# Kernel tuning notes

Measured on AMD Instinct MI355X. Metric: run time of the kernel, lower is better.

Reference implementation:

```python
import jax, jax.numpy as jnp
import numpy as np

N_NODES = 100000
N_EDGES = 600000
D = 128  # input_dim == output_dim (required by index_add into zeros_like(x) + residual)
EPS = 1e-5


def _linear_params(key, d_in, d_out):
    kw, kb = jax.random.split(key)
    bound = 1.0 / np.sqrt(d_in)
    w = jax.random.uniform(kw, (d_in, d_out), minval=-bound, maxval=bound, dtype=jnp.float32)
    b = jax.random.uniform(kb, (d_out,), minval=-bound, maxval=bound, dtype=jnp.float32)
    return w, b


def setup_inputs() -> dict:
    key = jax.random.key(0)
    ks = jax.random.split(key, 6)
    x = jax.random.normal(ks[0], (N_NODES, D), dtype=jnp.float32)
    edge_index = jax.random.randint(ks[1], (2, N_EDGES), 0, N_NODES, dtype=jnp.int32)
    w_m1, b_m1 = _linear_params(ks[2], 2 * D, D)
    w_m2, b_m2 = _linear_params(ks[3], D, D)
    w_u1, b_u1 = _linear_params(ks[4], 2 * D, D)
    w_u2, b_u2 = _linear_params(ks[5], D, D)
    gamma = jnp.ones((D,), dtype=jnp.float32)
    beta = jnp.zeros((D,), dtype=jnp.float32)
    return {
        "x": x, "edge_index": edge_index,
        "w_m1": w_m1, "b_m1": b_m1, "w_m2": w_m2, "b_m2": b_m2,
        "w_u1": w_u1, "b_u1": b_u1, "w_u2": w_u2, "b_u2": b_u2,
        "gamma": gamma, "beta": beta,
    }


def _layernorm(h, gamma, beta):
    mu = jnp.mean(h, axis=-1, keepdims=True)
    var = jnp.mean(jnp.square(h - mu), axis=-1, keepdims=True)
    return (h - mu) * jax.lax.rsqrt(var + EPS) * gamma + beta


def reference(x, edge_index, w_m1, b_m1, w_m2, b_m2, w_u1, b_u1, w_u2, b_u2, gamma, beta):
    row, col = edge_index[0], edge_index[1]
    # message MLP on concat of gathered endpoints: [E, 2D] -> [E, D]
    m_in = jnp.concatenate([x[row], x[col]], axis=-1)
    m = jax.nn.relu(m_in @ w_m1 + b_m1) @ w_m2 + b_m2
    # scatter-add messages to destination nodes (index_add along dim 0 with col)
    agg = jax.ops.segment_sum(m, col, num_segments=x.shape[0])
    # update MLP on [N, 2D] -> [N, D]
    u_in = jnp.concatenate([x, agg], axis=-1)
    h = jax.nn.relu(u_in @ w_u1 + b_u1) @ w_u2 + b_u2
    return _layernorm(h, gamma, beta) + x
```

## Files before the change

kernel.cpp:

```cpp
#include <hip/hip_runtime.h>
#include <hip/hip_bf16.h>
#include <stdint.h>

#define N_NODES 100000
#define N_EDGES 600000
#define D 128
#define EPS 1e-5f
#define SCAN_BS 512

typedef __attribute__((ext_vector_type(8))) short short8;
typedef __attribute__((ext_vector_type(16))) float floatx16;


__device__ __forceinline__ uint32_t pack_bf16_rne(float lo, float hi) {
    uint32_t ul = __builtin_bit_cast(uint32_t, lo);
    uint32_t uh = __builtin_bit_cast(uint32_t, hi);
    ul += 0x7fffu + ((ul >> 16) & 1u);
    uh += 0x7fffu + ((uh >> 16) & 1u);
    return (ul >> 16) | (uh & 0xffff0000u);
}

__device__ __forceinline__ unsigned short f32_to_bf16_rne(float f) {
    uint32_t u = __builtin_bit_cast(uint32_t, f);
    u += 0x7fffu + ((u >> 16) & 1u);
    return (unsigned short)(u >> 16);
}


__global__ void hist_kernel(const int* __restrict__ col, int* __restrict__ count) {
    int e = blockIdx.x * blockDim.x + threadIdx.x;
    if (e < N_EDGES) atomicAdd(&count[col[e]], 1);
}

__global__ void scanA_kernel(const int* __restrict__ count, int* __restrict__ base,
                             int* __restrict__ bsum) {
    __shared__ int tmp[SCAN_BS];
    int g = blockIdx.x * SCAN_BS + threadIdx.x;
    int v = (g < N_NODES) ? count[g] : 0;
    tmp[threadIdx.x] = v;
    __syncthreads();
    int acc = v;
#pragma unroll
    for (int off = 1; off < SCAN_BS; off <<= 1) {
        int add = (threadIdx.x >= off) ? tmp[threadIdx.x - off] : 0;
        __syncthreads();
        acc += add;
        tmp[threadIdx.x] = acc;
        __syncthreads();
    }
    if (g < N_NODES) base[g] = acc - v;
    if (threadIdx.x == SCAN_BS - 1) bsum[blockIdx.x] = acc;
}

__global__ void scanB_kernel(int* __restrict__ bsum, int nb) {
    __shared__ int tmp[256];
    int v = (threadIdx.x < nb) ? bsum[threadIdx.x] : 0;
    tmp[threadIdx.x] = v;
    __syncthreads();
    int acc = v;
#pragma unroll
    for (int off = 1; off < 256; off <<= 1) {
        int add = (threadIdx.x >= off) ? tmp[threadIdx.x - off] : 0;
        __syncthreads();
        acc += add;
        tmp[threadIdx.x] = acc;
        __syncthreads();
    }
    if (threadIdx.x < nb) bsum[threadIdx.x] = acc - v;
}

__global__ void scanC_kernel(int* __restrict__ base, const int* __restrict__ bsum,
                             int* __restrict__ cursor) {
    int g = blockIdx.x * SCAN_BS + threadIdx.x;
    if (g < N_NODES) {
        int b = base[g] + bsum[blockIdx.x];
        base[g] = b;
        cursor[g] = b;
    }
}

__global__ void scatter_kernel(const int* __restrict__ row, const int* __restrict__ col,
                               int* __restrict__ cursor, int* __restrict__ srow) {
    int e = blockIdx.x * blockDim.x + threadIdx.x;
    if (e < N_EDGES) {
        int p = atomicAdd(&cursor[col[e]], 1);
        srow[p] = row[e];
    }
}


__global__ void wc_kernel(const float* __restrict__ w2, const float* __restrict__ wu1,
                          float* __restrict__ wc) {
    int idx = blockIdx.x * blockDim.x + threadIdx.x;
    if (idx >= 128 * 128) return;
    int i = idx >> 7, n = idx & 127;
    float s = 0.0f;
    for (int k = 0; k < 128; ++k) s += w2[i * 128 + k] * wu1[(128 + k) * 128 + n];
    wc[idx] = s;
}

__global__ void vb_kernel(const float* __restrict__ b2, const float* __restrict__ wu1,
                          float* __restrict__ vb) {
    int n = threadIdx.x;
    if (n < 128) {
        float s = 0.0f;
        for (int k = 0; k < 128; ++k) s += b2[k] * wu1[(128 + k) * 128 + n];
        vb[n] = s;
    }
}

__global__ void prep_weights(const float* __restrict__ w, unsigned short* __restrict__ out, int K) {
    int idx = blockIdx.x * blockDim.x + threadIdx.x;
    int total = K * 128;
    if (idx >= total) return;
    int j    = idx & 7;
    int lane = (idx >> 3) & 63;
    int t    = (idx >> 9) & 3;
    int s    = idx >> 11;
    int k = s * 16 + ((lane >> 5) << 3) + j;
    int n = t * 32 + (lane & 31);
    out[idx] = f32_to_bf16_rne(w[k * 128 + n]);
}

__launch_bounds__(256, 2)
__global__ void xform_kernel(const float* __restrict__ x, const short8* __restrict__ w1f,
                             const float* __restrict__ b1, unsigned short* __restrict__ xtb) {
    __shared__ __align__(16) short h1[4][32 * 136];
    const int wave = threadIdx.x >> 6;
    const int lane = threadIdx.x & 63;
    const int l31  = lane & 31;
    const int half = lane >> 5;
    short* hl = h1[wave];

    const int nbase = (blockIdx.x * 4 + wave) * 32;
    const int n = min(nbase + l31, N_NODES - 1);
    const float* px = x + (size_t)n * D + half * 8;

    union { short8 v; uint32_t u[4]; } fa[8];
#pragma unroll
    for (int s = 0; s < 8; ++s) {
        const int off = s * 16;
        float4 a0 = *(const float4*)(px + off);
        float4 a1 = *(const float4*)(px + off + 4);
        fa[s].u[0] = pack_bf16_rne(a0.x, a0.y); fa[s].u[1] = pack_bf16_rne(a0.z, a0.w);
        fa[s].u[2] = pack_bf16_rne(a1.x, a1.y); fa[s].u[3] = pack_bf16_rne(a1.z, a1.w);
    }

#pragma unroll
    for (int p = 0; p < 2; ++p) {
        floatx16 acc[4];
#pragma unroll
        for (int t = 0; t < 4; ++t) acc[t] = (floatx16)0.0f;
#pragma unroll
        for (int s = 0; s < 8; ++s) {
#pragma unroll
            for (int t = 0; t < 4; ++t) {
                short8 wf = w1f[((p * 8 + s) * 4 + t) * 64 + lane];
                acc[t] = __builtin_amdgcn_mfma_f32_32x32x16_bf16(fa[s].v, wf, acc[t], 0, 0, 0);
            }
        }
#pragma unroll
        for (int t = 0; t < 4; ++t) {
            float bias = p ? b1[t * 32 + l31] : 0.0f;
#pragma unroll
            for (int r = 0; r < 16; ++r) {
                int m = (r & 3) + 8 * (r >> 2) + 4 * half;
                hl[m * 136 + t * 32 + l31] = (short)f32_to_bf16_rne(acc[t][r] + bias);
            }
        }
#pragma unroll
        for (int it = 0; it < 8; ++it) {
            int off = it * 512 + lane * 8;
            int row = off >> 7;
            int col = off & 127;
            if (nbase + row < N_NODES) {
                short8 v = *(const short8*)(hl + row * 136 + col);
                *(short8*)(xtb + (size_t)(nbase + row) * 256 + p * 128 + col) = v;
            }
        }
    }
}

__launch_bounds__(256, 8)
__global__ void agg_kernel(const uint32_t* __restrict__ xtb32,
                           const int* __restrict__ srow,
                           const int* __restrict__ base, const int* __restrict__ count,
                           uint32_t* __restrict__ hsum) {
    const int node = blockIdx.x * 4 + (threadIdx.x >> 6);
    const int lane = threadIdx.x & 63;
    if (node >= N_NODES) return;

    const uint32_t xbu = xtb32[(size_t)node * 128 + 64 + lane];
    const float xb_lo = __builtin_bit_cast(float, xbu << 16);
    const float xb_hi = __builtin_bit_cast(float, xbu & 0xffff0000u);

    float s_lo = 0.0f, s_hi = 0.0f;
    int i = base[node];
    const int endi = i + count[node];
    for (; i + 1 < endi; i += 2) {
        int r0 = srow[i], r1 = srow[i + 1];
        uint32_t a0 = xtb32[(size_t)r0 * 128 + lane];
        uint32_t a1 = xtb32[(size_t)r1 * 128 + lane];
        s_lo += fmaxf(__builtin_bit_cast(float, a0 << 16) + xb_lo, 0.0f);
        s_hi += fmaxf(__builtin_bit_cast(float, a0 & 0xffff0000u) + xb_hi, 0.0f);
        s_lo += fmaxf(__builtin_bit_cast(float, a1 << 16) + xb_lo, 0.0f);
        s_hi += fmaxf(__builtin_bit_cast(float, a1 & 0xffff0000u) + xb_hi, 0.0f);
    }
    if (i < endi) {
        int r0 = srow[i];
        uint32_t a0 = xtb32[(size_t)r0 * 128 + lane];
        s_lo += fmaxf(__builtin_bit_cast(float, a0 << 16) + xb_lo, 0.0f);
        s_hi += fmaxf(__builtin_bit_cast(float, a0 & 0xffff0000u) + xb_hi, 0.0f);
    }
    hsum[(size_t)node * 64 + lane] = pack_bf16_rne(s_lo, s_hi);
}

__launch_bounds__(256, 4)
__global__ void upd_kernel(const float* __restrict__ x, const unsigned short* __restrict__ hsum,
                           const short8* __restrict__ wu1tf, const short8* __restrict__ wcf,
                           const short8* __restrict__ wu2f,
                           const float* __restrict__ b_u1, const float* __restrict__ vb,
                           const int* __restrict__ count,
                           const float* __restrict__ b_u2,
                           const float* __restrict__ gamma, const float* __restrict__ beta,
                           float* __restrict__ out) {
    __shared__ __align__(16) short h1[4][32 * 136];
    const int wave = threadIdx.x >> 6;
    const int lane = threadIdx.x & 63;
    const int l31  = lane & 31;
    const int half = lane >> 5;
    short* hl = h1[wave];

    const int nbase = (blockIdx.x * 4 + wave) * 32;
    const int n = min(nbase + l31, N_NODES - 1);

    const float* px = x + (size_t)n * D + half * 8;
    const unsigned short* ph = hsum + (size_t)n * D + half * 8;

    floatx16 acc[4];
#pragma unroll
    for (int t = 0; t < 4; ++t) acc[t] = (floatx16)0.0f;

#pragma unroll
    for (int s = 0; s < 16; ++s) {
        union { short8 v; uint32_t u[4]; } fa;
        const short8* bf;
        if (s < 8) {
            const int off = s * 16;
            float4 a0 = *(const float4*)(px + off);
            float4 a1 = *(const float4*)(px + off + 4);
            fa.u[0] = pack_bf16_rne(a0.x, a0.y); fa.u[1] = pack_bf16_rne(a0.z, a0.w);
            fa.u[2] = pack_bf16_rne(a1.x, a1.y); fa.u[3] = pack_bf16_rne(a1.z, a1.w);
            bf = wu1tf + (s * 4) * 64;
        } else {
            fa.v = *(const short8*)(ph + (s - 8) * 16);
            bf = wcf + ((s - 8) * 4) * 64;
        }
#pragma unroll
        for (int t = 0; t < 4; ++t) {
            short8 wf = bf[t * 64 + lane];
            acc[t] = __builtin_amdgcn_mfma_f32_32x32x16_bf16(fa.v, wf, acc[t], 0, 0, 0);
        }
    }

    float bu1[4], vbt[4];
#pragma unroll
    for (int t = 0; t < 4; ++t) {
        bu1[t] = b_u1[t * 32 + l31];
        vbt[t] = vb[t * 32 + l31];
    }

#pragma unroll
    for (int r = 0; r < 16; ++r) {
        int m = (r & 3) + 8 * (r >> 2) + 4 * half;
        float dg = (float)count[min(nbase + m, N_NODES - 1)];
#pragma unroll
        for (int t = 0; t < 4; ++t) {
            float v = fmaxf(acc[t][r] + bu1[t] + dg * vbt[t], 0.0f);
            hl[m * 136 + t * 32 + l31] = (short)f32_to_bf16_rne(v);
        }
    }

    floatx16 acc2[4];
#pragma unroll
    for (int t = 0; t < 4; ++t) acc2[t] = (floatx16)0.0f;

#pragma unroll
    for (int s = 0; s < 8; ++s) {
        short8 af = *(const short8*)(hl + l31 * 136 + s * 16 + half * 8);
#pragma unroll
        for (int t = 0; t < 4; ++t) {
            short8 wf = wu2f[(s * 4 + t) * 64 + lane];
            acc2[t] = __builtin_amdgcn_mfma_f32_32x32x16_bf16(af, wf, acc2[t], 0, 0, 0);
        }
    }

    float g4[4], be4[4], bias2[4];
#pragma unroll
    for (int t = 0; t < 4; ++t) {
        g4[t]    = gamma[t * 32 + l31];
        be4[t]   = beta[t * 32 + l31];
        bias2[t] = b_u2[t * 32 + l31];
    }

#pragma unroll
    for (int r = 0; r < 16; ++r) {
        float hv[4];
        float s1 = 0.0f, s2 = 0.0f;
#pragma unroll
        for (int t = 0; t < 4; ++t) {
            hv[t] = acc2[t][r] + bias2[t];
            s1 += hv[t];
            s2 += hv[t] * hv[t];
        }
#pragma unroll
        for (int mask = 1; mask < 32; mask <<= 1) {
            s1 += __shfl_xor(s1, mask);
            s2 += __shfl_xor(s2, mask);
        }
        float mean = s1 * (1.0f / 128.0f);
        float var  = s2 * (1.0f / 128.0f) - mean * mean;
        float rs   = rsqrtf(var + EPS);
        int m = (r & 3) + 8 * (r >> 2) + 4 * half;
        int node = nbase + m;
        if (node < N_NODES) {
            const float* xr = x + (size_t)node * D + l31;
            float* orow = out + (size_t)node * D + l31;
#pragma unroll
            for (int t = 0; t < 4; ++t) {
                float v = (hv[t] - mean) * rs * g4[t] + be4[t] + xr[t * 32];
                orow[t * 32] = v;
            }
        }
    }
}

extern "C" void kernel_launch(void* const* d_in, const int* in_sizes, int n_in,
                              void* d_out, int out_size, void* d_ws, size_t ws_size,
                              hipStream_t stream) {
    const float* x     = (const float*)d_in[0];
    const int*   edge  = (const int*)d_in[1];
    const float* w_m1  = (const float*)d_in[2];
    const float* b_m1  = (const float*)d_in[3];
    const float* w_m2  = (const float*)d_in[4];
    const float* b_m2  = (const float*)d_in[5];
    const float* w_u1  = (const float*)d_in[6];
    const float* b_u1  = (const float*)d_in[7];
    const float* w_u2  = (const float*)d_in[8];
    const float* b_u2  = (const float*)d_in[9];
    const float* gamma = (const float*)d_in[10];
    const float* beta  = (const float*)d_in[11];
    float* out = (float*)d_out;

    char* ws = (char*)d_ws;
    size_t off = 0;
    auto alloc = [&](size_t bytes) { void* p = ws + off; off = (off + bytes + 15) & ~(size_t)15; return p; };

    unsigned short* xtb   = (unsigned short*)alloc((size_t)N_NODES * 256 * 2);
    unsigned short* hsumB = (unsigned short*)alloc((size_t)N_NODES * D * 2);
    unsigned short* wm1f  = (unsigned short*)alloc(256 * 128 * 2);
    unsigned short* wu1tf = (unsigned short*)alloc(128 * 128 * 2);
    unsigned short* wcf   = (unsigned short*)alloc(128 * 128 * 2);
    unsigned short* wu2f  = (unsigned short*)alloc(128 * 128 * 2);
    float* wc    = (float*)alloc(128 * 128 * 4);
    float* vb    = (float*)alloc(128 * 4);
    int* count   = (int*)alloc((size_t)N_NODES * 4);
    int* base    = (int*)alloc((size_t)N_NODES * 4);
    int* cursor  = (int*)alloc((size_t)N_NODES * 4);
    int* bsum    = (int*)alloc(256 * 4);
    int* srow    = (int*)alloc((size_t)N_EDGES * 4);

    const int* rowi = edge;
    const int* coli = edge + N_EDGES;
    const int NB = (N_NODES + SCAN_BS - 1) / SCAN_BS;

    (void)hipMemsetAsync(count, 0, (size_t)N_NODES * 4, stream);

    prep_weights<<<(256 * 128 + 255) / 256, 256, 0, stream>>>(w_m1, wm1f, 256);
    prep_weights<<<(128 * 128 + 255) / 256, 256, 0, stream>>>(w_u1, wu1tf, 128);
    prep_weights<<<(128 * 128 + 255) / 256, 256, 0, stream>>>(w_u2, wu2f, 128);
    wc_kernel<<<(128 * 128 + 255) / 256, 256, 0, stream>>>(w_m2, w_u1, wc);
    vb_kernel<<<1, 128, 0, stream>>>(b_m2, w_u1, vb);
    prep_weights<<<(128 * 128 + 255) / 256, 256, 0, stream>>>(wc, wcf, 128);

    hist_kernel<<<(N_EDGES + 255) / 256, 256, 0, stream>>>(coli, count);
    scanA_kernel<<<NB, SCAN_BS, 0, stream>>>(count, base, bsum);
    scanB_kernel<<<1, 256, 0, stream>>>(bsum, NB);
    scanC_kernel<<<NB, SCAN_BS, 0, stream>>>(base, bsum, cursor);
    scatter_kernel<<<(N_EDGES + 255) / 256, 256, 0, stream>>>(rowi, coli, cursor, srow);

    xform_kernel<<<(N_NODES + 127) / 128, 256, 0, stream>>>(
        x, (const short8*)wm1f, b_m1, xtb);
    agg_kernel<<<(N_NODES + 3) / 4, 256, 0, stream>>>(
        (const uint32_t*)xtb, srow, base, count, (uint32_t*)hsumB);
    upd_kernel<<<(N_NODES + 127) / 128, 256, 0, stream>>>(
        x, hsumB, (const short8*)wu1tf, (const short8*)wcf, (const short8*)wu2f,
        b_u1, vb, count, b_u2, gamma, beta, out);
}
```

Measured before the change: 312.4 us.

## Fuse weight-prep kernels into one launch and batch edge index loads in aggregation

Six small weight-preparation launches (three bf16 swizzles, the combined W_m2·W_u1 product, its bf16 swizzle and the bias projection) become one kernel that writes the swizzled combined weights directly. This removes five launches and the fp32 intermediate buffer. The aggregation kernel now loads up to 64 source indices per wave in one coalesced read, broadcasts them with shuffles and unrolls the gather by four to keep more loads in flight. The xform launch bound is also raised to four blocks per SM, which may add register pressure.

```diff
diff --git a/kernel.cpp b/kernel.cpp
--- a/kernel.cpp
+++ b/kernel.cpp
@@ -25,6 +25,9 @@
     u += 0x7fffu + ((u >> 16) & 1u);
     return (unsigned short)(u >> 16);
 }
+
+__device__ __forceinline__ float bflo(uint32_t a) { return __builtin_bit_cast(float, a << 16); }
+__device__ __forceinline__ float bfhi(uint32_t a) { return __builtin_bit_cast(float, a & 0xffff0000u); }
 
 
 __global__ void hist_kernel(const int* __restrict__ col, int* __restrict__ count) {
@@ -88,41 +91,55 @@
     }
 }
 
-
-__global__ void wc_kernel(const float* __restrict__ w2, const float* __restrict__ wu1,
-                          float* __restrict__ wc) {
+__global__ void prep_all(const float* __restrict__ w_m1, const float* __restrict__ w_u1,
+                         const float* __restrict__ w_u2, const float* __restrict__ w_m2,
+                         const float* __restrict__ b_m2,
+                         unsigned short* __restrict__ wm1f, unsigned short* __restrict__ wu1tf,
+                         unsigned short* __restrict__ wu2f, unsigned short* __restrict__ wcf,
+                         float* __restrict__ vb) {
     int idx = blockIdx.x * blockDim.x + threadIdx.x;
-    if (idx >= 128 * 128) return;
-    int i = idx >> 7, n = idx & 127;
-    float s = 0.0f;
-    for (int k = 0; k < 128; ++k) s += w2[i * 128 + k] * wu1[(128 + k) * 128 + n];
-    wc[idx] = s;
-}
-
-__global__ void vb_kernel(const float* __restrict__ b2, const float* __restrict__ wu1,
-                          float* __restrict__ vb) {
-    int n = threadIdx.x;
-    if (n < 128) {
-        float s = 0.0f;
-        for (int k = 0; k < 128; ++k) s += b2[k] * wu1[(128 + k) * 128 + n];
-        vb[n] = s;
-    }
-}
-
-__global__ void prep_weights(const float* __restrict__ w, unsigned short* __restrict__ out, int K) {
-    int idx = blockIdx.x * blockDim.x + threadIdx.x;
-    int total = K * 128;
-    if (idx >= total) return;
-    int j    = idx & 7;
-    int lane = (idx >> 3) & 63;
-    int t    = (idx >> 9) & 3;
-    int s    = idx >> 11;
-    int k = s * 16 + ((lane >> 5) << 3) + j;
-    int n = t * 32 + (lane & 31);
-    out[idx] = f32_to_bf16_rne(w[k * 128 + n]);
-}
-
-__launch_bounds__(256, 2)
+    int i = idx, k, n;
+    {
+        int j    = i & 7;
+        int lane = (i >> 3) & 63;
+        int t    = (i >> 9) & 3;
+        int s    = i >> 11;
+        k = (s & 15) * 16 + ((lane >> 5) << 3) + j;
+        n = t * 32 + (lane & 31);
+    }
+    if (idx < 32768) {
+        int j = idx & 7, lane = (idx >> 3) & 63, t = (idx >> 9) & 3, s = idx >> 11;
+        int kk = s * 16 + ((lane >> 5) << 3) + j;
+        wm1f[idx] = f32_to_bf16_rne(w_m1[kk * 128 + t * 32 + (lane & 31)]);
+    } else if (idx < 49152) {
+        int ii = idx - 32768;
+        int j = ii & 7, lane = (ii >> 3) & 63, t = (ii >> 9) & 3, s = ii >> 11;
+        int kk = s * 16 + ((lane >> 5) << 3) + j;
+        wu1tf[ii] = f32_to_bf16_rne(w_u1[kk * 128 + t * 32 + (lane & 31)]);
+    } else if (idx < 65536) {
+        int ii = idx - 49152;
+        int j = ii & 7, lane = (ii >> 3) & 63, t = (ii >> 9) & 3, s = ii >> 11;
+        int kk = s * 16 + ((lane >> 5) << 3) + j;
+        wu2f[ii] = f32_to_bf16_rne(w_u2[kk * 128 + t * 32 + (lane & 31)]);
+    } else if (idx < 81920) {
+        int ii = idx - 65536;
+        int j = ii & 7, lane = (ii >> 3) & 63, t = (ii >> 9) & 3, s = ii >> 11;
+        int kk = s * 16 + ((lane >> 5) << 3) + j;
+        int nn = t * 32 + (lane & 31);
+        float acc = 0.0f;
+        for (int q = 0; q < 128; ++q)
+            acc += w_m2[kk * 128 + q] * w_u1[(128 + q) * 128 + nn];
+        wcf[ii] = f32_to_bf16_rne(acc);
+    } else if (idx < 82048) {
+        int nn = idx - 81920;
+        float acc = 0.0f;
+        for (int q = 0; q < 128; ++q)
+            acc += b_m2[q] * w_u1[(128 + q) * 128 + nn];
+        vb[nn] = acc;
+    }
+}
+
+__launch_bounds__(256, 4)
 __global__ void xform_kernel(const float* __restrict__ x, const short8* __restrict__ w1f,
                              const float* __restrict__ b1, unsigned short* __restrict__ xtb) {
     __shared__ __align__(16) short h1[4][32 * 136];
@@ -190,27 +207,47 @@
     const int lane = threadIdx.x & 63;
     if (node >= N_NODES) return;
 
+    const int b   = base[node];
+    const int deg = count[node];
+
     const uint32_t xbu = xtb32[(size_t)node * 128 + 64 + lane];
-    const float xb_lo = __builtin_bit_cast(float, xbu << 16);
-    const float xb_hi = __builtin_bit_cast(float, xbu & 0xffff0000u);
+    const float xb_lo = bflo(xbu);
+    const float xb_hi = bfhi(xbu);
 
     float s_lo = 0.0f, s_hi = 0.0f;
-    int i = base[node];
-    const int endi = i + count[node];
-    for (; i + 1 < endi; i += 2) {
-        int r0 = srow[i], r1 = srow[i + 1];
-        uint32_t a0 = xtb32[(size_t)r0 * 128 + lane];
-        uint32_t a1 = xtb32[(size_t)r1 * 128 + lane];
-        s_lo += fmaxf(__builtin_bit_cast(float, a0 << 16) + xb_lo, 0.0f);
-        s_hi += fmaxf(__builtin_bit_cast(float, a0 & 0xffff0000u) + xb_hi, 0.0f);
-        s_lo += fmaxf(__builtin_bit_cast(float, a1 << 16) + xb_lo, 0.0f);
-        s_hi += fmaxf(__builtin_bit_cast(float, a1 & 0xffff0000u) + xb_hi, 0.0f);
-    }
-    if (i < endi) {
-        int r0 = srow[i];
-        uint32_t a0 = xtb32[(size_t)r0 * 128 + lane];
-        s_lo += fmaxf(__builtin_bit_cast(float, a0 << 16) + xb_lo, 0.0f);
-        s_hi += fmaxf(__builtin_bit_cast(float, a0 & 0xffff0000u) + xb_hi, 0.0f);
+
+    for (int t0 = 0; t0 < deg; t0 += 64) {
+        const int nb = min(64, deg - t0);
+        int sr = (lane < nb) ? srow[b + t0 + lane] : 0;
+        int d = 0;
+        for (; d + 4 <= nb; d += 4) {
+            int r0 = __shfl(sr, d);
+            int r1 = __shfl(sr, d + 1);
+            int r2 = __shfl(sr, d + 2);
+            int r3 = __shfl(sr, d + 3);
+            uint32_t a0 = xtb32[(size_t)r0 * 128 + lane];
+            uint32_t a1 = xtb32[(size_t)r1 * 128 + lane];
+            uint32_t a2 = xtb32[(size_t)r2 * 128 + lane];
+            uint32_t a3 = xtb32[(size_t)r3 * 128 + lane];
+            s_lo += fmaxf(bflo(a0) + xb_lo, 0.0f); s_hi += fmaxf(bfhi(a0) + xb_hi, 0.0f);
+            s_lo += fmaxf(bflo(a1) + xb_lo, 0.0f); s_hi += fmaxf(bfhi(a1) + xb_hi, 0.0f);
+            s_lo += fmaxf(bflo(a2) + xb_lo, 0.0f); s_hi += fmaxf(bfhi(a2) + xb_hi, 0.0f);
+            s_lo += fmaxf(bflo(a3) + xb_lo, 0.0f); s_hi += fmaxf(bfhi(a3) + xb_hi, 0.0f);
+        }
+        if (d + 2 <= nb) {
+            int r0 = __shfl(sr, d);
+            int r1 = __shfl(sr, d + 1);
+            uint32_t a0 = xtb32[(size_t)r0 * 128 + lane];
+            uint32_t a1 = xtb32[(size_t)r1 * 128 + lane];
+            s_lo += fmaxf(bflo(a0) + xb_lo, 0.0f); s_hi += fmaxf(bfhi(a0) + xb_hi, 0.0f);
+            s_lo += fmaxf(bflo(a1) + xb_lo, 0.0f); s_hi += fmaxf(bfhi(a1) + xb_hi, 0.0f);
+            d += 2;
+        }
+        if (d < nb) {
+            int r0 = __shfl(sr, d);
+            uint32_t a0 = xtb32[(size_t)r0 * 128 + lane];
+            s_lo += fmaxf(bflo(a0) + xb_lo, 0.0f); s_hi += fmaxf(bfhi(a0) + xb_hi, 0.0f);
+        }
     }
     hsum[(size_t)node * 64 + lane] = pack_bf16_rne(s_lo, s_hi);
 }
@@ -362,7 +399,6 @@
     unsigned short* wu1tf = (unsigned short*)alloc(128 * 128 * 2);
     unsigned short* wcf   = (unsigned short*)alloc(128 * 128 * 2);
     unsigned short* wu2f  = (unsigned short*)alloc(128 * 128 * 2);
-    float* wc    = (float*)alloc(128 * 128 * 4);
     float* vb    = (float*)alloc(128 * 4);
     int* count   = (int*)alloc((size_t)N_NODES * 4);
     int* base    = (int*)alloc((size_t)N_NODES * 4);
@@ -376,12 +412,8 @@
 
     (void)hipMemsetAsync(count, 0, (size_t)N_NODES * 4, stream);
 
-    prep_weights<<<(256 * 128 + 255) / 256, 256, 0, stream>>>(w_m1, wm1f, 256);
-    prep_weights<<<(128 * 128 + 255) / 256, 256, 0, stream>>>(w_u1, wu1tf, 128);
-    prep_weights<<<(128 * 128 + 255) / 256, 256, 0, stream>>>(w_u2, wu2f, 128);
-    wc_kernel<<<(128 * 128 + 255) / 256, 256, 0, stream>>>(w_m2, w_u1, wc);
-    vb_kernel<<<1, 128, 0, stream>>>(b_m2, w_u1, vb);
-    prep_weights<<<(128 * 128 + 255) / 256, 256, 0, stream>>>(wc, wcf, 128);
+    prep_all<<<(82048 + 255) / 256, 256, 0, stream>>>(
+        w_m1, w_u1, w_u2, w_m2, b_m2, wm1f, wu1tf, wu2f, wcf, vb);
 
     hist_kernel<<<(N_EDGES + 255) / 256, 256, 0, stream>>>(coli, count);
     scanA_kernel<<<NB, SCAN_BS, 0, stream>>>(count, base, bsum);
```

Result: faster. 291.7 us (-6.6%).
